# Performance work log

Hardware: AMD Instinct MI355X
Metric: run time of the kernel (lower is better)

The kernel has to match this reference:

```python
import jax, jax.numpy as jnp
import numpy as np

T, B, D, H = 256, 64, 1024, 1024
G = D + H  # gate input dim (concat of x and hx)


def setup_inputs() -> dict:
    key = jax.random.key(0)
    ks = jax.random.split(key, 5)
    s1 = 1.0 / np.sqrt(G)
    s2 = 1.0 / np.sqrt(H)
    inputs = jax.random.normal(ks[0], (T, B, D), dtype=jnp.float32)
    # gate order along leading axis: forget, input, update, output
    W1 = jax.random.uniform(ks[1], (4, G, H), minval=-s1, maxval=s1, dtype=jnp.float32)
    b1 = jax.random.uniform(ks[2], (4, H), minval=-s1, maxval=s1, dtype=jnp.float32)
    W2 = jax.random.uniform(ks[3], (4, H, H), minval=-s2, maxval=s2, dtype=jnp.float32)
    b2 = jax.random.uniform(ks[4], (4, H), minval=-s2, maxval=s2, dtype=jnp.float32)
    return {"inputs": inputs, "W1": W1, "b1": b1, "W2": W2, "b2": b2}


def reference(inputs, W1, b1, W2, b2):
    # LSTM cell where each gate is: act(Linear2(Linear1(cat[x, h])))
    batch = inputs.shape[1]
    hx0 = jnp.zeros((batch, H), dtype=inputs.dtype)
    cx0 = jnp.zeros((batch, H), dtype=inputs.dtype)

    def step(carry, x):
        hx, cx = carry
        comb = jnp.concatenate([x, hx], axis=1)               # [B, G]
        pre = jnp.einsum('bd,gdh->gbh', comb, W1) + b1[:, None, :]  # [4,B,H]
        z = jnp.einsum('gbh,ghk->gbk', pre, W2) + b2[:, None, :]    # [4,B,H]
        f = jax.nn.sigmoid(z[0])
        i = jax.nn.sigmoid(z[1])
        g = jnp.tanh(z[2])
        o = jax.nn.sigmoid(z[3])
        cx = f * cx + i * g
        hx = o * jnp.tanh(cx)
        return (hx, cx), hx

    (hx, cx), outs = jax.lax.scan(step, (hx0, cx0), inputs)
    return outs, hx, cx
```

## Files before the change

kernel.cpp:

```cpp
#include <hip/hip_runtime.h>
#include <hip/hip_bf16.h>

#define TSTEPS 256
#define NBLK 256

typedef short bf16x8 __attribute__((ext_vector_type(8)));
typedef float f32x4 __attribute__((ext_vector_type(4)));

__device__ __forceinline__ unsigned short f2bf(float f) {
    union { float f; unsigned u; } v; v.f = f;
    unsigned r = v.u + 0x7FFFu + ((v.u >> 16) & 1u);
    return (unsigned short)(r >> 16);
}
__device__ __forceinline__ float bf2f(unsigned short s) {
    union { unsigned u; float f; } v; v.u = ((unsigned)s) << 16; return v.f;
}

__global__ void hq_marker(float* out) { out[0] = 12345.0f; }

__global__ void hq_transpose(const float* __restrict__ in, unsigned short* __restrict__ out) {
    __shared__ float tile[64][65];
    const int R = 1024, C = 1024;
    int r0 = blockIdx.y * 64, c0 = blockIdx.x * 64;
    const float* src = in + (long)blockIdx.z * R * C;
    unsigned short* dst = out + (long)blockIdx.z * R * C;
    int col = threadIdx.x & 63, rr = threadIdx.x >> 6;
#pragma unroll
    for (int i = 0; i < 16; ++i) {
        int row = rr + i * 4;
        tile[row][col] = src[(long)(r0 + row) * C + c0 + col];
    }
    __syncthreads();
#pragma unroll
    for (int i = 0; i < 16; ++i) {
        int row = rr + i * 4;
        dst[(long)(c0 + row) * R + r0 + col] = f2bf(tile[col][row]);
    }
}

__global__ void hq_beff(const unsigned short* __restrict__ w2t, const float* __restrict__ b1,
                        const float* __restrict__ b2, float* __restrict__ beff) {
    int g = blockIdx.y;
    int h = blockIdx.x * 256 + threadIdx.x;
    const unsigned short* row = w2t + ((long)(g * 1024 + h)) * 1024;
    float s = 0.f;
    for (int k = 0; k < 1024; k += 8) {
        bf16x8 v = *reinterpret_cast<const bf16x8*>(row + k);
#pragma unroll
        for (int j = 0; j < 8; ++j) s += bf2f((unsigned short)v[j]) * b1[g * 1024 + k + j];
    }
    beff[g * 1024 + h] = s + b2[g * 1024 + h];
}

__global__ void hq_weff(const unsigned short* __restrict__ w2t, const float* __restrict__ w1,
                        unsigned short* __restrict__ wefft) {
    __shared__ unsigned short atile[64][136];
    const int g = blockIdx.z;
    const int d0 = blockIdx.x * 64;
    const int h0 = blockIdx.y * 64;
    const int tid = threadIdx.x;
    const int w = tid >> 6, lane = tid & 63;
    const int fr = lane & 15, fq = lane >> 4;
    f32x4 acc[4] = {};
    const int drow = d0 + w * 16 + fr;
    const float* bsrc = w1 + ((long)g * 2048 + drow) * 1024;
    for (int kc = 0; kc < 8; ++kc) {
#pragma unroll
        for (int i = 0; i < 4; ++i) {
            int id = tid + i * 256;
            int row = id >> 4, c8 = id & 15;
            bf16x8 v = *reinterpret_cast<const bf16x8*>(
                w2t + ((long)(g * 1024 + h0 + row)) * 1024 + kc * 128 + c8 * 8);
            *reinterpret_cast<bf16x8*>(&atile[row][c8 * 8]) = v;
        }
        __syncthreads();
#pragma unroll
        for (int kk = 0; kk < 4; ++kk) {
            int kl = kk * 32 + fq * 8;
            int kg = kc * 128 + kl;
            float4 bA = *reinterpret_cast<const float4*>(bsrc + kg);
            float4 bB = *reinterpret_cast<const float4*>(bsrc + kg + 4);
            bf16x8 bfv;
            bfv[0] = (short)f2bf(bA.x); bfv[1] = (short)f2bf(bA.y);
            bfv[2] = (short)f2bf(bA.z); bfv[3] = (short)f2bf(bA.w);
            bfv[4] = (short)f2bf(bB.x); bfv[5] = (short)f2bf(bB.y);
            bfv[6] = (short)f2bf(bB.z); bfv[7] = (short)f2bf(bB.w);
#pragma unroll
            for (int mi = 0; mi < 4; ++mi) {
                bf16x8 af = *reinterpret_cast<const bf16x8*>(&atile[mi * 16 + fr][kl]);
                acc[mi] = __builtin_amdgcn_mfma_f32_16x16x32_bf16(af, bfv, acc[mi], 0, 0, 0);
            }
        }
        __syncthreads();
    }
#pragma unroll
    for (int mi = 0; mi < 4; ++mi)
#pragma unroll
        for (int r = 0; r < 4; ++r) {
            int h = h0 + mi * 16 + fq * 4 + r;
            int d = d0 + w * 16 + fr;
            wefft[((long)(g * 1024 + h)) * 2048 + d] = f2bf(acc[mi][r]);
        }
}

__global__ void hq_xconv(const float* __restrict__ x, unsigned short* __restrict__ xbf) {
    long i = (long)blockIdx.x * 256 + threadIdx.x;
    for (; i < 4194304L; i += 524288L) {
        float4 v = reinterpret_cast<const float4*>(x)[i];
        ushort4 o;
        o.x = f2bf(v.x); o.y = f2bf(v.y); o.z = f2bf(v.z); o.w = f2bf(v.w);
        reinterpret_cast<ushort4*>(xbf)[i] = o;
    }
}

__device__ __forceinline__ void coh_load_hx(const void* pa, const void* pb, bf16x8* af) {
    asm volatile(
        "global_load_dwordx4 %0, %[a], off sc0 sc1\n\t"
        "global_load_dwordx4 %1, %[a], off offset:64 sc0 sc1\n\t"
        "global_load_dwordx4 %2, %[a], off offset:128 sc0 sc1\n\t"
        "global_load_dwordx4 %3, %[a], off offset:192 sc0 sc1\n\t"
        "global_load_dwordx4 %4, %[b], off sc0 sc1\n\t"
        "global_load_dwordx4 %5, %[b], off offset:64 sc0 sc1\n\t"
        "global_load_dwordx4 %6, %[b], off offset:128 sc0 sc1\n\t"
        "global_load_dwordx4 %7, %[b], off offset:192 sc0 sc1\n\t"
        "s_waitcnt vmcnt(0)"
        : "=&v"(af[0]), "=&v"(af[1]), "=&v"(af[2]), "=&v"(af[3]),
          "=&v"(af[4]), "=&v"(af[5]), "=&v"(af[6]), "=&v"(af[7])
        : [a] "v"(pa), [b] "v"(pb)
        : "memory");
}
__device__ __forceinline__ unsigned coh_load_flag(const unsigned* p) {
    unsigned r;
    asm volatile(
        "global_load_dword %0, %[a], off sc0 sc1\n\t"
        "s_waitcnt vmcnt(0)"
        : "=&v"(r) : [a] "v"(p) : "memory");
    return r;
}
__device__ __forceinline__ void vm_drain() {
    asm volatile("s_waitcnt vmcnt(0)" ::: "memory");
}
__device__ __forceinline__ void lgkm_barrier() {
    asm volatile("s_waitcnt lgkmcnt(0)\n\ts_barrier" ::: "memory");
    __builtin_amdgcn_sched_barrier(0);
}

__global__ __launch_bounds__(1024, 4) void hq_seq(
    const unsigned short* __restrict__ xbf,
    const unsigned short* __restrict__ wefft,
    const float* __restrict__ beff,
    float* __restrict__ outs,
    float* __restrict__ hxf, float* __restrict__ cxf,
    unsigned short* __restrict__ hxbuf,
    unsigned* __restrict__ flags)
{
    __shared__ float zpart[16][2][32][16];
    __shared__ float hvbuf[256];
    __shared__ float cbuf[256];
    const int tid = threadIdx.x;
    const int lane = tid & 63, kq = tid >> 6;
    const int fr = lane & 15, fq = lane >> 4;
    const int bid = blockIdx.x;
    const int bq = bid >> 7, cb = bid & 127;
    const int b0 = bq * 32, ho = cb * 8;
    const int k0 = kq * 128;

    bf16x8 breg[2][4];
#pragma unroll
    for (int nt = 0; nt < 2; ++nt) {
        const int col = nt * 16 + fr;
        const int g = col >> 3, hl = col & 7;
        const unsigned short* wrow = wefft + ((long)(g * 1024 + ho + hl)) * 2048 + k0 + fq * 8;
#pragma unroll
        for (int s = 0; s < 4; ++s) breg[nt][s] = *(const bf16x8*)(wrow + s * 32);
    }

    const int eb = tid >> 3, ehl = tid & 7;
    float creg = 0.f;
    float be[4] = {0.f, 0.f, 0.f, 0.f};
    if (tid < 256) {
#pragma unroll
        for (int g = 0; g < 4; ++g) be[g] = beff[g * 1024 + ho + ehl];
    }

    const unsigned* my_flag = flags + bq * 128 + ((kq - 8) & 7) * 16 + fr;

    bf16x8 af[8];
    if (kq < 8) {
        const unsigned short* p0 = xbf + ((long)(b0 + fr)) * 1024 + k0 + fq * 8;
        const unsigned short* p1 = p0 + 16 * 1024;
#pragma unroll
        for (int s = 0; s < 4; ++s) {
            af[s]     = *(const bf16x8*)(p0 + s * 32);
            af[4 + s] = *(const bf16x8*)(p1 + s * 32);
        }
    }

    for (int t = 0; t < TSTEPS; ++t) {
        if (kq >= 8) {
            if (t == 0) {
#pragma unroll
                for (int i = 0; i < 8; ++i) af[i] = (bf16x8){0, 0, 0, 0, 0, 0, 0, 0};
            } else {
                for (int g = 0; g < (1 << 16); ++g) {
                    unsigned v = coh_load_flag(my_flag);
                    if (__all(v >= (unsigned)t)) break;
                }
                const unsigned short* hx_r = hxbuf + (t & 1) * 65536;
                const char* pa = (const char*)(hx_r + ((long)(b0 + fr)) * 1024 + (k0 - 1024) + fq * 8);
                const char* pb = pa + 32768;
                coh_load_hx(pa, pb, af);
            }
        }

        f32x4 acc[2][2] = {};
#pragma unroll
        for (int s = 0; s < 4; ++s)
#pragma unroll
            for (int mt = 0; mt < 2; ++mt)
#pragma unroll
                for (int nt = 0; nt < 2; ++nt)
                    acc[mt][nt] = __builtin_amdgcn_mfma_f32_16x16x32_bf16(
                        af[mt * 4 + s], breg[nt][s], acc[mt][nt], 0, 0, 0);

#pragma unroll
        for (int mt = 0; mt < 2; ++mt)
#pragma unroll
            for (int nt = 0; nt < 2; ++nt) {
                const int col = nt * 16 + fr;
                const int prow = (fq * 4) ^ ((col & 3) << 2);
                *(f32x4*)&zpart[kq][mt][col][prow] = acc[mt][nt];
            }
        lgkm_barrier();

        if (tid < 256) {
            const int emt = eb >> 4, erow = eb & 15;
            float z[4];
#pragma unroll
            for (int g = 0; g < 4; ++g) {
                const int col = g * 8 + ehl;
                const int pr = erow ^ ((col & 3) << 2);
                float s = be[g];
#pragma unroll
                for (int q = 0; q < 16; ++q) s += zpart[q][emt][col][pr];
                z[g] = s;
            }
            float fg = 1.f / (1.f + __expf(-z[0]));
            float ig = 1.f / (1.f + __expf(-z[1]));
            float gg = 2.f / (1.f + __expf(-2.f * z[2])) - 1.f;
            float og = 1.f / (1.f + __expf(-z[3]));
            creg = fg * creg + ig * gg;
            float hv = og * (2.f / (1.f + __expf(-2.f * creg)) - 1.f);
            const int b = b0 + eb, h = ho + ehl;
            hvbuf[tid] = hv;
            if (t == TSTEPS - 1) cbuf[tid] = creg;

            unsigned hb = (unsigned)f2bf(hv);
            unsigned ob = (unsigned)__shfl_xor((int)hb, 1);
            if ((tid & 1) == 0) {
                unsigned pack = (hb & 0xFFFFu) | (ob << 16);
                unsigned* hx_w = (unsigned*)(hxbuf + ((t + 1) & 1) * 65536 + b * 1024 + h);
                __hip_atomic_store(hx_w, pack, __ATOMIC_RELAXED, __HIP_MEMORY_SCOPE_AGENT);
            }
            vm_drain();
        }
        lgkm_barrier();
        if (tid == 0)
            __hip_atomic_store(flags + bid, (unsigned)(t + 1), __ATOMIC_RELAXED,
                               __HIP_MEMORY_SCOPE_AGENT);
        if (kq < 8 && t + 1 < TSTEPS) {
            const unsigned short* p0 = xbf + ((long)((t + 1) * 64 + b0 + fr)) * 1024 + k0 + fq * 8;
            const unsigned short* p1 = p0 + 16 * 1024;
#pragma unroll
            for (int s = 0; s < 4; ++s) {
                af[s]     = *(const bf16x8*)(p0 + s * 32);
                af[4 + s] = *(const bf16x8*)(p1 + s * 32);
            }
        }
        if (tid >= 768) {
            const int et = tid - 768;
            const int b = b0 + (et >> 3), h = ho + (et & 7);
            float hv = hvbuf[et];
            outs[((long)(t * 64 + b)) * 1024 + h] = hv;
            if (t == TSTEPS - 1) { hxf[b * 1024 + h] = hv; cxf[b * 1024 + h] = cbuf[et]; }
        }
    }
}

extern "C" void kernel_launch(void* const* d_in, const int* in_sizes, int n_in,
                              void* d_out, int out_size, void* d_ws, size_t ws_size,
                              hipStream_t stream) {
    (void)in_sizes; (void)n_in; (void)out_size;
    const float* x  = (const float*)d_in[0];
    const float* W1 = (const float*)d_in[1];
    const float* b1 = (const float*)d_in[2];
    const float* W2 = (const float*)d_in[3];
    const float* b2 = (const float*)d_in[4];
    float* outs = (float*)d_out;
    float* hxf = outs + 16777216L;
    float* cxf = hxf + 65536;

    const size_t off_wefft = 0;
    const size_t off_xbf   = 16777216;
    const size_t off_w2t   = off_xbf;
    const size_t off_hx    = 50331648;
    const size_t off_beff  = 50593792;
    const size_t off_flags = 50610176;
    const size_t need      = 50611200;
    if (ws_size < need) { hq_marker<<<1, 1, 0, stream>>>((float*)d_out); return; }

    char* ws = (char*)d_ws;
    unsigned short* wefft = (unsigned short*)(ws + off_wefft);
    unsigned short* xbf   = (unsigned short*)(ws + off_xbf);
    unsigned short* w2t   = (unsigned short*)(ws + off_w2t);
    unsigned short* hxbuf = (unsigned short*)(ws + off_hx);
    float* beff = (float*)(ws + off_beff);
    unsigned* flags = (unsigned*)(ws + off_flags);

    hipMemsetAsync(ws + off_flags, 0, 1024, stream);
    hq_transpose<<<dim3(16, 16, 4), 256, 0, stream>>>(W2, w2t);
    hq_beff<<<dim3(4, 4), 256, 0, stream>>>(w2t, b1, b2, beff);
    hq_weff<<<dim3(32, 16, 4), 256, 0, stream>>>(w2t, W1, wefft);
    hq_xconv<<<2048, 256, 0, stream>>>(x, xbf);

    const unsigned short* xbf_c = xbf;
    const unsigned short* wefft_c = wefft;
    const float* beff_c = beff;
    void* args[] = { (void*)&xbf_c, (void*)&wefft_c, (void*)&beff_c,
                     (void*)&outs, (void*)&hxf, (void*)&cxf,
                     (void*)&hxbuf, (void*)&flags };
    hipError_t ce = hipLaunchCooperativeKernel((const void*)hq_seq, dim3(NBLK), dim3(1024),
                                               args, 0, stream);
    if (ce != hipSuccess) {
        hq_seq<<<NBLK, 1024, 0, stream>>>(xbf, wefft, beff, outs, hxf, cxf, hxbuf, flags);
    }
}
```

Before: 1.482 ms.

## Remap block-to-tile assignment and use acquire fence with plain hx loads

Changes how block IDs map to batch-half and column tiles, interleaving the two batch halves across adjacent blocks, and indexes the flag array by logical tile so the readiness flags stay consistent. The inline-asm system-coherent (sc0 sc1) hx loads are replaced with an agent-scope acquire fence followed by ordinary vector loads. This lets the compiler schedule the loads and may let them hit in cache. Correctness now depends on the fence giving visibility of other blocks' atomic stores, and the remap changes which blocks share XCDs and caches.

```diff
diff --git a/kernel.cpp b/kernel.cpp
--- a/kernel.cpp
+++ b/kernel.cpp
@@ -113,22 +113,6 @@
     }
 }
 
-__device__ __forceinline__ void coh_load_hx(const void* pa, const void* pb, bf16x8* af) {
-    asm volatile(
-        "global_load_dwordx4 %0, %[a], off sc0 sc1\n\t"
-        "global_load_dwordx4 %1, %[a], off offset:64 sc0 sc1\n\t"
-        "global_load_dwordx4 %2, %[a], off offset:128 sc0 sc1\n\t"
-        "global_load_dwordx4 %3, %[a], off offset:192 sc0 sc1\n\t"
-        "global_load_dwordx4 %4, %[b], off sc0 sc1\n\t"
-        "global_load_dwordx4 %5, %[b], off offset:64 sc0 sc1\n\t"
-        "global_load_dwordx4 %6, %[b], off offset:128 sc0 sc1\n\t"
-        "global_load_dwordx4 %7, %[b], off offset:192 sc0 sc1\n\t"
-        "s_waitcnt vmcnt(0)"
-        : "=&v"(af[0]), "=&v"(af[1]), "=&v"(af[2]), "=&v"(af[3]),
-          "=&v"(af[4]), "=&v"(af[5]), "=&v"(af[6]), "=&v"(af[7])
-        : [a] "v"(pa), [b] "v"(pb)
-        : "memory");
-}
 __device__ __forceinline__ unsigned coh_load_flag(const unsigned* p) {
     unsigned r;
     asm volatile(
@@ -161,9 +145,11 @@
     const int lane = tid & 63, kq = tid >> 6;
     const int fr = lane & 15, fq = lane >> 4;
     const int bid = blockIdx.x;
-    const int bq = bid >> 7, cb = bid & 127;
+    const int bq = (bid >> 1) & 1;
+    const int cb = (bid & 1) | ((bid >> 2) << 1);
     const int b0 = bq * 32, ho = cb * 8;
     const int k0 = kq * 128;
+    const int flidx = bq * 128 + cb;
 
     bf16x8 breg[2][4];
 #pragma unroll
@@ -206,10 +192,15 @@
                     unsigned v = coh_load_flag(my_flag);
                     if (__all(v >= (unsigned)t)) break;
                 }
+                __builtin_amdgcn_fence(__ATOMIC_ACQUIRE, "agent");
                 const unsigned short* hx_r = hxbuf + (t & 1) * 65536;
-                const char* pa = (const char*)(hx_r + ((long)(b0 + fr)) * 1024 + (k0 - 1024) + fq * 8);
-                const char* pb = pa + 32768;
-                coh_load_hx(pa, pb, af);
+                const bf16x8* q0 = (const bf16x8*)(hx_r + ((long)(b0 + fr)) * 1024 + (k0 - 1024) + fq * 8);
+                const bf16x8* q1 = q0 + 2048;
+#pragma unroll
+                for (int s = 0; s < 4; ++s) {
+                    af[s]     = q0[s * 4];
+                    af[4 + s] = q1[s * 4];
+                }
             }
         }
 
@@ -266,7 +257,7 @@
         }
         lgkm_barrier();
         if (tid == 0)
-            __hip_atomic_store(flags + bid, (unsigned)(t + 1), __ATOMIC_RELAXED,
+            __hip_atomic_store(flags + flidx, (unsigned)(t + 1), __ATOMIC_RELAXED,
                                __HIP_MEMORY_SCOPE_AGENT);
         if (kq < 8 && t + 1 < TSTEPS) {
             const unsigned short* p0 = xbf + ((long)((t + 1) * 64 + b0 + fr)) * 1024 + k0 + fq * 8;
```

Measured after the change: 4.684 ms. +216.0%, slower.
